# Kernel tuning notes

Measured on AMD Instinct MI355X. Metric: run time of the kernel, lower is better.

## Reference

```python
import jax, jax.numpy as jnp
import numpy as np

N_USERS = 2213
N_SOURCES = 50000
D = 128
H = 8
BATCH = 1024


def setup_inputs() -> dict:
    key = jax.random.key(0)
    k1, k2, k3, k4, k5, k6 = jax.random.split(key, 6)
    X_user_id = jax.random.randint(k1, (BATCH,), 0, N_USERS)
    user_emb = jax.random.normal(k2, (N_USERS, D), dtype=jnp.float32)
    source_emb = jax.random.normal(k3, (N_SOURCES, D), dtype=jnp.float32)
    Wcm = jax.random.normal(k4, (H, D, D), dtype=jnp.float32) * 0.05
    W1 = jax.random.normal(k5, (H * D, D), dtype=jnp.float32) * 0.05
    A_us = jax.random.uniform(k6, (N_USERS, N_SOURCES), dtype=jnp.float32)
    return {"X_user_id": X_user_id, "user_emb": user_emb, "source_emb": source_emb,
            "Wcm": Wcm, "W1": W1, "A_us": A_us}


def reference(X_user_id, user_emb, source_emb, Wcm, W1, A_us):
    d = user_emb.shape[-1]
    scale = jnp.sqrt(jnp.asarray(d, dtype=user_emb.dtype))
    Xu = user_emb[X_user_id]            # [b, d]
    A = A_us[X_user_id]                 # [b, S] dense adjacency rows
    M = source_emb                      # [S, d]
    n_heads = Wcm.shape[0]
    m_hat = []
    for i in range(n_heads):            # small fixed head loop (keeps [b,S] peak memory per head)
        scores = jnp.einsum('bd,de,se->bs', Xu, Wcm[i], M) / scale
        scores = jax.nn.relu(scores)
        alpha = jax.nn.softmax(scores * A, axis=-1)   # dropout is identity in eval
        m_hat.append(alpha @ M)         # [b, d]
    m = jnp.concatenate(m_hat, axis=-1) @ W1          # [b, d]
    user_rep = jax.nn.elu(m) + Xu
    return user_rep
```

## Files before the change

### kernel.cpp

```cpp
#include <hip/hip_runtime.h>
#include <hip/hip_bf16.h>
#include <math.h>


#define S_TOT 50000
#define S_PAD 50304
#define DDIM 128
#define NHEAD 8
#define NB 1024
#define BQ 32
#define SN 32
#define NCH 16
#define SCHUNK 3136
#define NIT (SCHUNK / SN)
#define NBT 32
#define PAD_CNT 176.0f

typedef __bf16 v8bf __attribute__((ext_vector_type(8)));
typedef float v4f __attribute__((ext_vector_type(4)));

union U4BF { uint4 u; v8bf b; };

__device__ inline unsigned short f2bf(float f) {
  union { float f; unsigned u; } v; v.f = f;
  unsigned r = (v.u + 0x7FFFu + ((v.u >> 16) & 1u)) >> 16;
  return (unsigned short)r;
}

__global__ void k_qproj(const int* __restrict__ uid, const float* __restrict__ user_emb,
                        const float* __restrict__ Wcm, unsigned short* __restrict__ Qbf) {
  int bh = blockIdx.x;
  int b = bh >> 3, h = bh & 7;
  int e = threadIdx.x;
  int u = uid[b];
  const float* xu = user_emb + (long)u * DDIM;
  const float* w = Wcm + (long)h * DDIM * DDIM + e;
  float acc = 0.f;
#pragma unroll 16
  for (int d = 0; d < DDIM; ++d) acc += xu[d] * w[(long)d * DDIM];
  Qbf[(long)bh * DDIM + e] = f2bf(acc * 0.08838834764831845f);
}

__global__ void k_prepM(const float* __restrict__ M, unsigned short* __restrict__ Mbf,
                        unsigned short* __restrict__ MbfT) {
  __shared__ unsigned short tile[64][66];
  int s0 = blockIdx.x * 64, d0 = blockIdx.y * 64;
  int t = threadIdx.x;
#pragma unroll
  for (int it = 0; it < 16; ++it) {
    int flat = t + 256 * it;
    int sl = flat >> 6, dl = flat & 63;
    int s = s0 + sl;
    float v = (s < S_TOT) ? M[(long)s * DDIM + d0 + dl] : 0.f;
    unsigned short bb = f2bf(v);
    tile[sl][dl] = bb;
    Mbf[(long)s * DDIM + d0 + dl] = bb;
  }
  __syncthreads();
#pragma unroll
  for (int it = 0; it < 16; ++it) {
    int flat = t + 256 * it;
    int dl = flat >> 6, sl = flat & 63;
    MbfT[(long)(d0 + dl) * S_PAD + s0 + sl] = tile[sl][dl];
  }
}

__launch_bounds__(512, 4)
__global__ void k_attn(const int* __restrict__ uid_g, const float* __restrict__ A_us,
                       const unsigned short* __restrict__ Qbf,
                       const unsigned short* __restrict__ Mbf,
                       const unsigned short* __restrict__ MbfT,
                       unsigned short* __restrict__ part_acc, float* __restrict__ part_sum) {
  __shared__ __align__(16) unsigned short lds_M[2][SN][136];
  __shared__ __align__(16) unsigned short lds_Mt[2][DDIM][40];
  __shared__ __align__(16) unsigned short lds_P[256][40];
  __shared__ __align__(16) float lds_At[2][SN][36];
  __shared__ int lds_uid[BQ];

  const int ch = blockIdx.x;
  const int bt = blockIdx.y;
  const int tid = threadIdx.x;
  const int w = tid >> 6;
  const int lane = tid & 63;
  const int q = lane >> 4, li = lane & 15;

  if (tid < BQ) lds_uid[tid] = uid_g[bt * BQ + tid];

  U4BF qf[2][4];
#pragma unroll
  for (int mt = 0; mt < 2; ++mt)
#pragma unroll
    for (int k = 0; k < 4; ++k) {
      int b = bt * BQ + mt * 16 + li;
      qf[mt][k].u = *(const uint4*)(Qbf + ((long)(b * NHEAD + w) * DDIM + k * 32 + q * 8));
    }

  v4f zero4 = {0.f, 0.f, 0.f, 0.f};
  v4f acc[2][8];
#pragma unroll
  for (int mt = 0; mt < 2; ++mt)
#pragma unroll
    for (int dt = 0; dt < 8; ++dt) acc[mt][dt] = zero4;
  float sE[2][4] = {{0.f,0.f,0.f,0.f},{0.f,0.f,0.f,0.f}};

  __syncthreads();

  const int s_beg = ch * SCHUNK;

  auto stage = [&](int buf, int s0) {
    int sl = tid >> 4, d = (tid & 15) * 8;
    *(uint4*)&lds_M[buf][sl][d] = *(const uint4*)(Mbf + (long)(s0 + sl) * DDIM + d);
    int dd = tid >> 2, pp = (tid & 3) * 8;
    *(uint4*)&lds_Mt[buf][dd][pp] = *(const uint4*)(MbfT + (long)dd * S_PAD + s0 + pp);
    if (tid < 256) {
      int bl = tid >> 3, sq = (tid & 7) * 4;
      const float* arow = A_us + (long)lds_uid[bl] * S_TOT;
      int sg = s0 + sq;
      float4 av;
      if (sg + 3 < S_TOT) {
        av = *(const float4*)(arow + sg);
      } else {
        av.x = (sg + 0 < S_TOT) ? arow[sg + 0] : 0.f;
        av.y = (sg + 1 < S_TOT) ? arow[sg + 1] : 0.f;
        av.z = (sg + 2 < S_TOT) ? arow[sg + 2] : 0.f;
        av.w = (sg + 3 < S_TOT) ? arow[sg + 3] : 0.f;
      }
      lds_At[buf][sq + 0][bl] = av.x;
      lds_At[buf][sq + 1][bl] = av.y;
      lds_At[buf][sq + 2][bl] = av.z;
      lds_At[buf][sq + 3][bl] = av.w;
    }
  };

  stage(0, s_beg);
  __syncthreads();

  for (int it = 0; it < NIT; ++it) {
    const int p = it & 1;
    const int s0 = s_beg + it * SN;
    if (it + 1 < NIT) stage(1 - p, s0 + SN);

    U4BF bfm[2][4];
#pragma unroll
    for (int nt = 0; nt < 2; ++nt)
#pragma unroll
      for (int k = 0; k < 4; ++k)
        bfm[nt][k].u = *(const uint4*)&lds_M[p][nt * 16 + li][k * 32 + q * 8];

    v4f c[2][2];
    c[0][0] = zero4; c[0][1] = zero4; c[1][0] = zero4; c[1][1] = zero4;
#pragma unroll
    for (int k = 0; k < 4; ++k)
#pragma unroll
      for (int mt = 0; mt < 2; ++mt)
#pragma unroll
        for (int nt = 0; nt < 2; ++nt)
          c[mt][nt] = __builtin_amdgcn_mfma_f32_16x16x32_bf16(qf[mt][k].b, bfm[nt][k].b, c[mt][nt], 0, 0, 0);

#pragma unroll
    for (int mt = 0; mt < 2; ++mt)
#pragma unroll
      for (int nt = 0; nt < 2; ++nt) {
        int sloc = nt * 16 + li;
        const float4 a4 = *(const float4*)&lds_At[p][sloc][mt * 16 + q * 4];
        float aarr[4] = {a4.x, a4.y, a4.z, a4.w};
#pragma unroll
        for (int r = 0; r < 4; ++r) {
          float sc = fmaxf(c[mt][nt][r], 0.f) * aarr[r];
          float pv = __expf(sc);
          sE[mt][r] += pv;
          lds_P[w * 32 + mt * 16 + q * 4 + r][sloc] =
              (unsigned short)(__float_as_uint(pv) >> 16);
        }
      }
    __syncthreads();

    U4BF pf[2];
#pragma unroll
    for (int mt = 0; mt < 2; ++mt)
      pf[mt].u = *(const uint4*)&lds_P[w * 32 + mt * 16 + li][q * 8];
#pragma unroll
    for (int dt = 0; dt < 8; ++dt) {
      U4BF mf;
      mf.u = *(const uint4*)&lds_Mt[p][dt * 16 + li][q * 8];
#pragma unroll
      for (int mt = 0; mt < 2; ++mt)
        acc[mt][dt] = __builtin_amdgcn_mfma_f32_16x16x32_bf16(pf[mt].b, mf.b, acc[mt][dt], 0, 0, 0);
    }
    __syncthreads();
  }

  long base = ((long)ch * NBT + bt) * 256;
#pragma unroll
  for (int mt = 0; mt < 2; ++mt)
#pragma unroll
    for (int dt = 0; dt < 8; ++dt)
#pragma unroll
      for (int r = 0; r < 4; ++r) {
        int m = w * 32 + mt * 16 + q * 4 + r;
        part_acc[(base + m) * DDIM + dt * 16 + li] = f2bf(acc[mt][dt][r]);
      }
#pragma unroll
  for (int mt = 0; mt < 2; ++mt)
#pragma unroll
    for (int r = 0; r < 4; ++r) {
      float v = sE[mt][r];
      v += __shfl_xor(v, 1);
      v += __shfl_xor(v, 2);
      v += __shfl_xor(v, 4);
      v += __shfl_xor(v, 8);
      if (li == 0) part_sum[base + w * 32 + mt * 16 + q * 4 + r] = v;
    }
}

__global__ void k_reduce(const unsigned short* __restrict__ part_acc,
                         const float* __restrict__ part_sum, float* __restrict__ hhat) {
  int g = blockIdx.x * 256 + threadIdx.x;
  int bt = g >> 15;
  int m = (g >> 7) & 255;
  int e = g & 127;
  float a = 0.f, s = 0.f;
#pragma unroll
  for (int ch = 0; ch < NCH; ++ch) {
    long base = ((long)ch * NBT + bt) * 256 + m;
    unsigned ub = part_acc[base * DDIM + e];
    a += __uint_as_float(ub << 16);
    s += part_sum[base];
  }
  s -= PAD_CNT;
  int h = m >> 5, bl = m & 31;
  int b = bt * BQ + bl;
  hhat[(long)b * 1024 + h * DDIM + e] = a / s;
}

__global__ void k_final(const float* __restrict__ hhat, const float* __restrict__ W1,
                        const int* __restrict__ uid, const float* __restrict__ user_emb,
                        float* __restrict__ out) {
  int blk = blockIdx.x;
  int d = threadIdx.x & 127;
  int half = threadIdx.x >> 7;
  int b0 = blk * 4 + half * 2;
  float a0 = 0.f, a1 = 0.f;
  const float* h0 = hhat + (long)b0 * 1024;
  const float* h1 = h0 + 1024;
#pragma unroll 8
  for (int k = 0; k < 1024; ++k) {
    float wv = W1[(long)k * DDIM + d];
    a0 += h0[k] * wv;
    a1 += h1[k] * wv;
  }
  float e0 = (a0 > 0.f) ? a0 : expm1f(a0);
  float e1 = (a1 > 0.f) ? a1 : expm1f(a1);
  out[(long)b0 * DDIM + d]         = e0 + user_emb[(long)uid[b0] * DDIM + d];
  out[(long)(b0 + 1) * DDIM + d]   = e1 + user_emb[(long)uid[b0 + 1] * DDIM + d];
}

extern "C" void kernel_launch(void* const* d_in, const int* in_sizes, int n_in,
                              void* d_out, int out_size, void* d_ws, size_t ws_size,
                              hipStream_t stream) {
  const int* uid        = (const int*)d_in[0];
  const float* user_emb = (const float*)d_in[1];
  const float* src_emb  = (const float*)d_in[2];
  const float* Wcm      = (const float*)d_in[3];
  const float* W1       = (const float*)d_in[4];
  const float* A_us     = (const float*)d_in[5];
  float* out = (float*)d_out;

  char* ws = (char*)d_ws;
  unsigned short* Qbf      = (unsigned short*)(ws + 0);
  unsigned short* Mbf      = (unsigned short*)(ws + 2097152);
  unsigned short* MbfT     = (unsigned short*)(ws + 14974976);
  unsigned short* part_acc = (unsigned short*)(ws + 27852800);
  float* part_sum          = (float*)(ws + 61407232);
  float* hhat              = (float*)(ws + 61931520);

  k_qproj<<<dim3(NB * NHEAD), dim3(128), 0, stream>>>(uid, user_emb, Wcm, Qbf);
  k_prepM<<<dim3(S_PAD / 64, DDIM / 64), dim3(256), 0, stream>>>(src_emb, Mbf, MbfT);
  k_attn<<<dim3(NCH, NBT), dim3(512), 0, stream>>>(uid, A_us, Qbf, Mbf, MbfT, part_acc, part_sum);
  k_reduce<<<dim3(NBT * 256 * DDIM / 256), dim3(256), 0, stream>>>(part_acc, part_sum, hhat);
  k_final<<<dim3(256), dim3(256), 0, stream>>>(hhat, W1, uid, user_emb, out);
}
```

Before: 1.078 ms.

## Use direct global-to-LDS loads with swizzled layouts, batch qproj, reshape final GEMV

The attention kernel now stages M and M^T tiles with global_load_lds (direct global-to-LDS DMA) into XOR-swizzled, unpadded LDS layouts. It issues the A-row loads early and writes them to LDS after compute, drops one barrier per iteration, and raises wave priority around the MFMA blocks. The query projection now processes 16 users per block, sharing Wcm loads through LDS-cached user rows. The final GEMV uses one batch row per 128 threads with 512-thread blocks. Together these aim to cut LDS bank conflicts, register staging traffic and sync overhead. Removing the barrier between writing and reading lds_P is only safe if each wave reads back only its own rows, which the indexing appears to ensure.

```diff
diff --git a/kernel.cpp b/kernel.cpp
--- a/kernel.cpp
+++ b/kernel.cpp
@@ -27,18 +27,34 @@
   return (unsigned short)r;
 }
 
+__device__ __forceinline__ void glld16(const void* g, void* l) {
+  __builtin_amdgcn_global_load_lds((const __attribute__((address_space(1))) void*)g,
+                                   (__attribute__((address_space(3))) void*)l, 16, 0, 0);
+}
+
 __global__ void k_qproj(const int* __restrict__ uid, const float* __restrict__ user_emb,
                         const float* __restrict__ Wcm, unsigned short* __restrict__ Qbf) {
-  int bh = blockIdx.x;
-  int b = bh >> 3, h = bh & 7;
+  __shared__ float xu[16][DDIM];
+  int h = blockIdx.x & 7, g = blockIdx.x >> 3;
   int e = threadIdx.x;
-  int u = uid[b];
-  const float* xu = user_emb + (long)u * DDIM;
-  const float* w = Wcm + (long)h * DDIM * DDIM + e;
-  float acc = 0.f;
-#pragma unroll 16
-  for (int d = 0; d < DDIM; ++d) acc += xu[d] * w[(long)d * DDIM];
-  Qbf[(long)bh * DDIM + e] = f2bf(acc * 0.08838834764831845f);
+#pragma unroll
+  for (int i = 0; i < 16; ++i)
+    xu[i][e] = user_emb[(long)uid[(g << 4) + i] * DDIM + e];
+  __syncthreads();
+  float acc[16];
+#pragma unroll
+  for (int i = 0; i < 16; ++i) acc[i] = 0.f;
+  const float* wp = Wcm + (long)h * DDIM * DDIM + e;
+#pragma unroll 4
+  for (int d = 0; d < DDIM; ++d) {
+    float wv = wp[(long)d * DDIM];
+#pragma unroll
+    for (int i = 0; i < 16; ++i) acc[i] += xu[i][d] * wv;
+  }
+#pragma unroll
+  for (int i = 0; i < 16; ++i)
+    Qbf[((long)((g << 4) + i) * NHEAD + h) * DDIM + e] =
+        f2bf(acc[i] * 0.08838834764831845f);
 }
 
 __global__ void k_prepM(const float* __restrict__ M, unsigned short* __restrict__ Mbf,
@@ -71,8 +87,8 @@
                        const unsigned short* __restrict__ Mbf,
                        const unsigned short* __restrict__ MbfT,
                        unsigned short* __restrict__ part_acc, float* __restrict__ part_sum) {
-  __shared__ __align__(16) unsigned short lds_M[2][SN][136];
-  __shared__ __align__(16) unsigned short lds_Mt[2][DDIM][40];
+  __shared__ __align__(16) unsigned short lds_M[2][SN][DDIM];
+  __shared__ __align__(16) unsigned short lds_Mt[2][4][DDIM][8];
   __shared__ __align__(16) unsigned short lds_P[256][40];
   __shared__ __align__(16) float lds_At[2][SN][36];
   __shared__ int lds_uid[BQ];
@@ -105,18 +121,26 @@
 
   __syncthreads();
 
+  const int abl = tid >> 3, asq = (tid & 7) * 4;
+  const float* arow = nullptr;
+  if (tid < 256) arow = A_us + (long)lds_uid[abl] * S_TOT;
+
   const int s_beg = ch * SCHUNK;
 
-  auto stage = [&](int buf, int s0) {
-    int sl = tid >> 4, d = (tid & 15) * 8;
-    *(uint4*)&lds_M[buf][sl][d] = *(const uint4*)(Mbf + (long)(s0 + sl) * DDIM + d);
-    int dd = tid >> 2, pp = (tid & 3) * 8;
-    *(uint4*)&lds_Mt[buf][dd][pp] = *(const uint4*)(MbfT + (long)dd * S_PAD + s0 + pp);
+  auto mstage = [&](int buf, int s0) {
+    {
+      int srow = (w << 2) + (lane >> 4);
+      int c16 = (lane & 15) ^ (srow & 7);
+      glld16(Mbf + (long)(s0 + srow) * DDIM + (c16 << 3), &lds_M[buf][w << 2][0]);
+    }
+    {
+      int qg = w >> 1, d0 = (w & 1) << 6;
+      glld16(MbfT + (long)(d0 + lane) * S_PAD + s0 + (qg << 3), &lds_Mt[buf][qg][d0][0]);
+    }
+  };
+  auto aload = [&](int s0, float4& av) {
     if (tid < 256) {
-      int bl = tid >> 3, sq = (tid & 7) * 4;
-      const float* arow = A_us + (long)lds_uid[bl] * S_TOT;
-      int sg = s0 + sq;
-      float4 av;
+      int sg = s0 + asq;
       if (sg + 3 < S_TOT) {
         av = *(const float4*)(arow + sg);
       } else {
@@ -125,68 +149,87 @@
         av.z = (sg + 2 < S_TOT) ? arow[sg + 2] : 0.f;
         av.w = (sg + 3 < S_TOT) ? arow[sg + 3] : 0.f;
       }
-      lds_At[buf][sq + 0][bl] = av.x;
-      lds_At[buf][sq + 1][bl] = av.y;
-      lds_At[buf][sq + 2][bl] = av.z;
-      lds_At[buf][sq + 3][bl] = av.w;
     }
   };
-
-  stage(0, s_beg);
+  auto awrite = [&](int buf, const float4& av) {
+    if (tid < 256) {
+      lds_At[buf][asq + 0][abl] = av.x;
+      lds_At[buf][asq + 1][abl] = av.y;
+      lds_At[buf][asq + 2][abl] = av.z;
+      lds_At[buf][asq + 3][abl] = av.w;
+    }
+  };
+
+  {
+    float4 av = {0.f, 0.f, 0.f, 0.f};
+    mstage(0, s_beg);
+    aload(s_beg, av);
+    awrite(0, av);
+  }
   __syncthreads();
 
   for (int it = 0; it < NIT; ++it) {
     const int p = it & 1;
     const int s0 = s_beg + it * SN;
-    if (it + 1 < NIT) stage(1 - p, s0 + SN);
-
-    U4BF bfm[2][4];
-#pragma unroll
-    for (int nt = 0; nt < 2; ++nt)
-#pragma unroll
-      for (int k = 0; k < 4; ++k)
-        bfm[nt][k].u = *(const uint4*)&lds_M[p][nt * 16 + li][k * 32 + q * 8];
+    float4 avn = {0.f, 0.f, 0.f, 0.f};
+    if (it + 1 < NIT) {
+      mstage(1 - p, s0 + SN);
+      aload(s0 + SN, avn);
+    }
 
     v4f c[2][2];
     c[0][0] = zero4; c[0][1] = zero4; c[1][0] = zero4; c[1][1] = zero4;
-#pragma unroll
-    for (int k = 0; k < 4; ++k)
-#pragma unroll
-      for (int mt = 0; mt < 2; ++mt)
-#pragma unroll
-        for (int nt = 0; nt < 2; ++nt)
-          c[mt][nt] = __builtin_amdgcn_mfma_f32_16x16x32_bf16(qf[mt][k].b, bfm[nt][k].b, c[mt][nt], 0, 0, 0);
+    __builtin_amdgcn_s_setprio(1);
+#pragma unroll
+    for (int k = 0; k < 4; ++k) {
+      U4BF b0, b1;
+      int r0 = li, r1 = 16 + li;
+      b0.u = *(const uint4*)&lds_M[p][r0][(((k << 2) + q) ^ (r0 & 7)) << 3];
+      b1.u = *(const uint4*)&lds_M[p][r1][(((k << 2) + q) ^ (r1 & 7)) << 3];
+      c[0][0] = __builtin_amdgcn_mfma_f32_16x16x32_bf16(qf[0][k].b, b0.b, c[0][0], 0, 0, 0);
+      c[0][1] = __builtin_amdgcn_mfma_f32_16x16x32_bf16(qf[0][k].b, b1.b, c[0][1], 0, 0, 0);
+      c[1][0] = __builtin_amdgcn_mfma_f32_16x16x32_bf16(qf[1][k].b, b0.b, c[1][0], 0, 0, 0);
+      c[1][1] = __builtin_amdgcn_mfma_f32_16x16x32_bf16(qf[1][k].b, b1.b, c[1][1], 0, 0, 0);
+    }
+    __builtin_amdgcn_s_setprio(0);
 
 #pragma unroll
     for (int mt = 0; mt < 2; ++mt)
 #pragma unroll
       for (int nt = 0; nt < 2; ++nt) {
         int sloc = nt * 16 + li;
-        const float4 a4 = *(const float4*)&lds_At[p][sloc][mt * 16 + q * 4];
+        const float4 a4 = *(const float4*)&lds_At[p][sloc][(mt << 4) + (q << 2)];
         float aarr[4] = {a4.x, a4.y, a4.z, a4.w};
+        int pcol = sloc ^ (q << 3);
+        int prow = (w << 5) + (mt << 4) + (q << 2);
 #pragma unroll
         for (int r = 0; r < 4; ++r) {
           float sc = fmaxf(c[mt][nt][r], 0.f) * aarr[r];
           float pv = __expf(sc);
           sE[mt][r] += pv;
-          lds_P[w * 32 + mt * 16 + q * 4 + r][sloc] =
+          lds_P[prow + r][pcol] =
               (unsigned short)(__float_as_uint(pv) >> 16);
         }
       }
-    __syncthreads();
 
     U4BF pf[2];
-#pragma unroll
-    for (int mt = 0; mt < 2; ++mt)
-      pf[mt].u = *(const uint4*)&lds_P[w * 32 + mt * 16 + li][q * 8];
+    {
+      int xq = (q ^ ((li >> 2) & 3)) << 3;
+      pf[0].u = *(const uint4*)&lds_P[(w << 5) + li][xq];
+      pf[1].u = *(const uint4*)&lds_P[(w << 5) + 16 + li][xq];
+    }
+    __builtin_amdgcn_s_setprio(1);
 #pragma unroll
     for (int dt = 0; dt < 8; ++dt) {
       U4BF mf;
-      mf.u = *(const uint4*)&lds_Mt[p][dt * 16 + li][q * 8];
-#pragma unroll
-      for (int mt = 0; mt < 2; ++mt)
-        acc[mt][dt] = __builtin_amdgcn_mfma_f32_16x16x32_bf16(pf[mt].b, mf.b, acc[mt][dt], 0, 0, 0);
-    }
+      mf.u = *(const uint4*)&lds_Mt[p][q][dt * 16 + li][0];
+      acc[0][dt] = __builtin_amdgcn_mfma_f32_16x16x32_bf16(pf[0].b, mf.b, acc[0][dt], 0, 0, 0);
+      acc[1][dt] = __builtin_amdgcn_mfma_f32_16x16x32_bf16(pf[1].b, mf.b, acc[1][dt], 0, 0, 0);
+    }
+    __builtin_amdgcn_s_setprio(0);
+
+    if (it + 1 < NIT) awrite(1 - p, avn);
+
     __syncthreads();
   }
 
@@ -236,23 +279,16 @@
 __global__ void k_final(const float* __restrict__ hhat, const float* __restrict__ W1,
                         const int* __restrict__ uid, const float* __restrict__ user_emb,
                         float* __restrict__ out) {
-  int blk = blockIdx.x;
   int d = threadIdx.x & 127;
-  int half = threadIdx.x >> 7;
-  int b0 = blk * 4 + half * 2;
-  float a0 = 0.f, a1 = 0.f;
-  const float* h0 = hhat + (long)b0 * 1024;
-  const float* h1 = h0 + 1024;
+  int sub = threadIdx.x >> 7;
+  int b = (blockIdx.x << 2) + sub;
+  const float* hr = hhat + (long)b * 1024;
+  float a = 0.f;
 #pragma unroll 8
-  for (int k = 0; k < 1024; ++k) {
-    float wv = W1[(long)k * DDIM + d];
-    a0 += h0[k] * wv;
-    a1 += h1[k] * wv;
-  }
-  float e0 = (a0 > 0.f) ? a0 : expm1f(a0);
-  float e1 = (a1 > 0.f) ? a1 : expm1f(a1);
-  out[(long)b0 * DDIM + d]         = e0 + user_emb[(long)uid[b0] * DDIM + d];
-  out[(long)(b0 + 1) * DDIM + d]   = e1 + user_emb[(long)uid[b0 + 1] * DDIM + d];
+  for (int k = 0; k < 1024; ++k)
+    a += hr[k] * W1[(long)k * DDIM + d];
+  float e = (a > 0.f) ? a : expm1f(a);
+  out[(long)b * DDIM + d] = e + user_emb[(long)uid[b] * DDIM + d];
 }
 
 extern "C" void kernel_launch(void* const* d_in, const int* in_sizes, int n_in,
@@ -274,9 +310,9 @@
   float* part_sum          = (float*)(ws + 61407232);
   float* hhat              = (float*)(ws + 61931520);
 
-  k_qproj<<<dim3(NB * NHEAD), dim3(128), 0, stream>>>(uid, user_emb, Wcm, Qbf);
+  k_qproj<<<dim3(NB / 16 * NHEAD), dim3(128), 0, stream>>>(uid, user_emb, Wcm, Qbf);
   k_prepM<<<dim3(S_PAD / 64, DDIM / 64), dim3(256), 0, stream>>>(src_emb, Mbf, MbfT);
   k_attn<<<dim3(NCH, NBT), dim3(512), 0, stream>>>(uid, A_us, Qbf, Mbf, MbfT, part_acc, part_sum);
   k_reduce<<<dim3(NBT * 256 * DDIM / 256), dim3(256), 0, stream>>>(part_acc, part_sum, hhat);
-  k_final<<<dim3(256), dim3(256), 0, stream>>>(hhat, W1, uid, user_emb, out);
-}
+  k_final<<<dim3(256), dim3(512), 0, stream>>>(hhat, W1, uid, user_emb, out);
+}
```

Result: slower. 1.285 ms (+19.2%).
